# Kernel tuning notes

Hardware: AMD Instinct MI355X
Metric: run time of the kernel (lower is better)

The kernel has to match this reference:

```python
import jax, jax.numpy as jnp
import numpy as np

B, P, D = 8, 1024, 768
H = 12
HD = D // H


def setup_inputs() -> dict:
    key = jax.random.key(0)
    k1, k2, k3, k4, k5 = jax.random.split(key, 5)
    s = 0.02
    return {
        "x": jax.random.normal(k1, (B, P, D), dtype=jnp.float32),
        "w_qkv": jax.random.normal(k2, (D, 3 * D), dtype=jnp.float32) * s,
        "b_qkv": jax.random.normal(k3, (3 * D,), dtype=jnp.float32) * s,
        "w_proj": jax.random.normal(k4, (D, D), dtype=jnp.float32) * s,
        "b_proj": jax.random.normal(k5, (D,), dtype=jnp.float32) * s,
    }


def reference(x, w_qkv, b_qkv, w_proj, b_proj):
    b, p, d = x.shape
    scale = HD ** -0.5
    qkv = x @ w_qkv + b_qkv                      # [B,P,3D]
    qkv = qkv.reshape(b, p, 3, H, HD).transpose(2, 0, 3, 1, 4)  # [3,B,H,P,HD]
    q, k, v = qkv[0], qkv[1], qkv[2]
    attn = jnp.einsum("bhqd,bhkd->bhqk", q, k) * scale
    attn = jax.nn.softmax(attn, axis=-1)         # attn_drop is identity (p=0)
    weighted_avg = jnp.einsum("bhqk,bhkd->bhqd", attn, v)
    weighted_avg = weighted_avg.transpose(0, 2, 1, 3).reshape(b, p, d)  # [B,P,D]
    out = weighted_avg @ w_proj + b_proj         # proj_drop is identity (p=0)
    return (out, weighted_avg)
```

## Files before the change

### kernel.cpp

```cpp
#include <hip/hip_runtime.h>
#include <hip/hip_bf16.h>


typedef __attribute__((ext_vector_type(8))) short short8;
typedef __attribute__((ext_vector_type(4))) float f32x4;

#define MFMA_BF16(a, b, c) __builtin_amdgcn_mfma_f32_16x16x32_bf16((a), (b), (c), 0, 0, 0)

#define NB 8
#define NP 1024
#define ND 768
#define NH 12
#define NHD 64
#define NTOK (NB * NP)
#define N3D (3 * ND)
#define OUT_HALF (NTOK * ND)
#define QSCALE 0.18033688f

__device__ __forceinline__ void gload_lds16(const void* gptr, void* ldsptr) {
  __builtin_amdgcn_global_load_lds(
      (const __attribute__((address_space(1))) unsigned int*)gptr,
      (__attribute__((address_space(3))) unsigned int*)ldsptr, 16, 0, 0);
}


__global__ void k_cvt_x(const float* __restrict__ in, __hip_bfloat16* __restrict__ out) {
  int i = (blockIdx.x * 256 + threadIdx.x) * 8;
  float4 a = *(const float4*)(in + i);
  float4 b = *(const float4*)(in + i + 4);
  union { __hip_bfloat16 h[8]; uint4 u; } r;
  r.h[0] = __float2bfloat16(a.x); r.h[1] = __float2bfloat16(a.y);
  r.h[2] = __float2bfloat16(a.z); r.h[3] = __float2bfloat16(a.w);
  r.h[4] = __float2bfloat16(b.x); r.h[5] = __float2bfloat16(b.y);
  r.h[6] = __float2bfloat16(b.z); r.h[7] = __float2bfloat16(b.w);
  *(uint4*)(out + i) = r.u;
}

__global__ void k_cvt_t(const float* __restrict__ in, __hip_bfloat16* __restrict__ out,
                        int K, int N) {
  __shared__ float tile[32][33];
  int k0 = blockIdx.x * 32;
  int n0 = blockIdx.y * 32;
  int r = threadIdx.x >> 5;
  int c = threadIdx.x & 31;
#pragma unroll
  for (int i = 0; i < 4; ++i)
    tile[r + 8 * i][c] = in[(size_t)(k0 + r + 8 * i) * N + n0 + c];
  __syncthreads();
#pragma unroll
  for (int i = 0; i < 4; ++i)
    out[(size_t)(n0 + r + 8 * i) * K + k0 + c] = __float2bfloat16(tile[c][r + 8 * i]);
}


__device__ __forceinline__ void gemm_mainloop(const __hip_bfloat16* __restrict__ A,
                                              const __hip_bfloat16* __restrict__ BT,
                                              int K, int m0, int n0,
                                              __hip_bfloat16* As, __hip_bfloat16* Bs,
                                              f32x4 acc[4][4]) {
  const int tid = threadIdx.x;
  const int wid = tid >> 6, lane = tid & 63;
  const int wm = wid >> 1, wn = wid & 1;
  const int lrow = lane & 15, lk = lane >> 4;

  const int nkt = K / 32;

#define STAGE_G(kt, half)                                                \
  {                                                                      \
    const int k0s = (kt) * 32;                                           \
    _Pragma("unroll")                                                    \
    for (int t = 0; t < 2; ++t) {                                        \
      int o = (tid + t * 256) * 16;        \
      int mr = o >> 6;                    \
      int kk = (o & 63) >> 1;                   \
      gload_lds16(A + (size_t)(m0 + mr) * K + k0s + kk,                  \
                  (char*)As + (half) * 8192 + wid * 1024 + t * 4096);    \
      gload_lds16(BT + (size_t)(n0 + mr) * K + k0s + kk,                 \
                  (char*)Bs + (half) * 8192 + wid * 1024 + t * 4096);    \
    }                                                                    \
  }

  STAGE_G(0, 0);
  __syncthreads();

  for (int kt = 0; kt < nkt; ++kt) {
    const int cur = kt & 1;
    if (kt + 1 < nkt) STAGE_G(kt + 1, cur ^ 1);

    short8 af[4], bf[4];
#pragma unroll
    for (int i = 0; i < 4; ++i) {
      af[i] = *(const short8*)((const char*)As + cur * 8192 +
                               (wm * 64 + i * 16 + lrow) * 64 + lk * 16);
      bf[i] = *(const short8*)((const char*)Bs + cur * 8192 +
                               (wn * 64 + i * 16 + lrow) * 64 + lk * 16);
    }
#pragma unroll
    for (int mi = 0; mi < 4; ++mi)
#pragma unroll
      for (int ni = 0; ni < 4; ++ni)
        acc[mi][ni] = MFMA_BF16(af[mi], bf[ni], acc[mi][ni]);

    __syncthreads();
  }
#undef STAGE_G
}


__launch_bounds__(256)
__global__ void k_qkv_gemm(const __hip_bfloat16* __restrict__ A,
                           const __hip_bfloat16* __restrict__ BT,
                           const float* __restrict__ bias,
                           __hip_bfloat16* __restrict__ q_ws,
                           __hip_bfloat16* __restrict__ k_ws,
                           __hip_bfloat16* __restrict__ v_ws) {
  __shared__ __hip_bfloat16 As[2 * 128 * 32];
  __shared__ __hip_bfloat16 Bs[2 * 128 * 32];
  const int mt = blockIdx.x & 63, nt = blockIdx.x >> 6;
  const int m0 = mt * 128, n0 = nt * 128;
  const int wid = threadIdx.x >> 6, lane = threadIdx.x & 63;
  const int wm = wid >> 1, wn = wid & 1;
  const int lrow = lane & 15, lk = lane >> 4;

  f32x4 acc[4][4] = {};
  gemm_mainloop(A, BT, ND, m0, n0, As, Bs, acc);

  const int which = n0 / ND;
#pragma unroll
  for (int ni = 0; ni < 4; ++ni) {
    const int n = n0 + wn * 64 + ni * 16 + lrow;
    const float bv = bias[n];
    const int hh = (n % ND) >> 6;
    const int hd = n & 63;
#pragma unroll
    for (int mi = 0; mi < 4; ++mi) {
      const int mbase = m0 + wm * 64 + mi * 16 + lk * 4;
#pragma unroll
      for (int i = 0; i < 4; ++i) {
        const int m = mbase + i;
        const float v = acc[mi][ni][i] + bv;
        const int b = m >> 10, p = m & 1023;
        const int bh = b * NH + hh;
        if (which == 0)      q_ws[((size_t)bh * NP + p) * NHD + hd] = __float2bfloat16(v * QSCALE);
        else if (which == 1) k_ws[((size_t)bh * NP + p) * NHD + hd] = __float2bfloat16(v);
        else                 v_ws[((size_t)bh * NHD + hd) * NP + p] = __float2bfloat16(v);
      }
    }
  }
}


#define KVBLK 64

__launch_bounds__(256)
__global__ void k_attn(const __hip_bfloat16* __restrict__ q_ws,
                       const __hip_bfloat16* __restrict__ k_ws,
                       const __hip_bfloat16* __restrict__ v_ws,
                       float* __restrict__ wavg_f32,
                       __hip_bfloat16* __restrict__ wavg_bf) {
  __shared__ char smem[2 * 16384 + 4 * 2304];
  const int bh = blockIdx.y;
  const int tid = threadIdx.x;
  const int wid = tid >> 6, lane = tid & 63;
  const int lrow = lane & 15, lk = lane >> 4;
  const int q0 = blockIdx.x * 64 + wid * 16;
  char* pbuf = smem + 32768 + wid * 2304;

  const __hip_bfloat16* Qb = q_ws + (size_t)bh * NP * NHD;
  const __hip_bfloat16* Kb = k_ws + (size_t)bh * NP * NHD;
  const __hip_bfloat16* Vb = v_ws + (size_t)bh * NHD * NP;

  short8 qf0 = *(const short8*)(Qb + (size_t)(q0 + lrow) * NHD + lk * 8);
  short8 qf1 = *(const short8*)(Qb + (size_t)(q0 + lrow) * NHD + 32 + lk * 8);

  f32x4 acc[4] = {};
  float dsum[4] = {0.f, 0.f, 0.f, 0.f};

#define STAGE(buf, key0)                                                          \
  {                                                                               \
    _Pragma("unroll")                                                             \
    for (int p = 0; p < 2; ++p) {                                                 \
      const int L = p * 4096 + tid * 16;                                          \
      const int r = L >> 7;                                                       \
      const int cb = L & 127;                                                     \
      const int sc = (cb ^ ((r & 7) << 4)) >> 1;        \
      gload_lds16(Kb + (size_t)((key0) + r) * NHD + sc, (buf) + L);               \
      gload_lds16(Vb + (size_t)r * NP + (key0) + sc, (buf) + 8192 + L);           \
    }                                                                             \
  }

  char* cur = smem;
  char* nxt = smem + 16384;
  STAGE(cur, 0);
  __syncthreads();

  for (int kc = 0; kc < NP / KVBLK; ++kc) {
    if (kc < NP / KVBLK - 1) STAGE(nxt, (kc + 1) * KVBLK);

    char* Ks = cur;
    char* Vs = cur + 8192;

    f32x4 s[4];
#pragma unroll
    for (int kt = 0; kt < 4; ++kt) {
      const int row = kt * 16 + lrow;
      const int sw = (row & 7) << 4;
      short8 klo = *(const short8*)(Ks + row * 128 + ((lk * 16) ^ sw));
      short8 khi = *(const short8*)(Ks + row * 128 + ((64 + lk * 16) ^ sw));
      f32x4 z = {0.f, 0.f, 0.f, 0.f};
      s[kt] = MFMA_BF16(qf0, klo, z);
      s[kt] = MFMA_BF16(qf1, khi, s[kt]);
    }

#pragma unroll
    for (int kt = 0; kt < 4; ++kt)
#pragma unroll
      for (int i = 0; i < 4; ++i) {
        const float p = exp2f(s[kt][i]);
        dsum[i] += p;
        *(__hip_bfloat16*)(pbuf + (lk * 4 + i) * 144 + kt * 32 + lrow * 2) =
            __float2bfloat16(p);
      }

#pragma unroll
    for (int kh = 0; kh < 2; ++kh) {
      short8 a2 = *(const short8*)(pbuf + lrow * 144 + kh * 64 + lk * 16);
#pragma unroll
      for (int hdt = 0; hdt < 4; ++hdt) {
        const int row = hdt * 16 + lrow;
        short8 vf = *(const short8*)(Vs + row * 128 +
                                     ((kh * 64 + lk * 16) ^ ((row & 7) << 4)));
        acc[hdt] = MFMA_BF16(a2, vf, acc[hdt]);
      }
    }

    __syncthreads();
    char* t = cur; cur = nxt; nxt = t;
  }

#pragma unroll
  for (int i = 0; i < 4; ++i) {
#pragma unroll
    for (int off = 1; off < 16; off <<= 1)
      dsum[i] += __shfl_xor(dsum[i], off, 16);
  }
  float rd[4];
#pragma unroll
  for (int i = 0; i < 4; ++i) rd[i] = 1.0f / dsum[i];

  const int b = bh / NH, hh = bh % NH;
#pragma unroll
  for (int hdt = 0; hdt < 4; ++hdt) {
#pragma unroll
    for (int i = 0; i < 4; ++i) {
      const int qq = q0 + lk * 4 + i;
      const int col = hh * NHD + hdt * 16 + lrow;
      const float val = acc[hdt][i] * rd[i];
      const size_t o = ((size_t)b * NP + qq) * ND + col;
      wavg_f32[o] = val;
      wavg_bf[o] = __float2bfloat16(val);
    }
  }
#undef STAGE
}


__launch_bounds__(256)
__global__ void k_proj_gemm(const __hip_bfloat16* __restrict__ A,
                            const __hip_bfloat16* __restrict__ BT,
                            const float* __restrict__ bias,
                            float* __restrict__ C) {
  __shared__ __hip_bfloat16 As[2 * 128 * 32];
  __shared__ __hip_bfloat16 Bs[2 * 128 * 32];
  const int mt = blockIdx.x & 63, nt = blockIdx.x >> 6;
  const int m0 = mt * 128, n0 = nt * 128;
  const int wid = threadIdx.x >> 6, lane = threadIdx.x & 63;
  const int wm = wid >> 1, wn = wid & 1;
  const int lrow = lane & 15, lk = lane >> 4;

  f32x4 acc[4][4] = {};
  gemm_mainloop(A, BT, ND, m0, n0, As, Bs, acc);

#pragma unroll
  for (int ni = 0; ni < 4; ++ni) {
    const int n = n0 + wn * 64 + ni * 16 + lrow;
    const float bv = bias[n];
#pragma unroll
    for (int mi = 0; mi < 4; ++mi) {
      const int mbase = m0 + wm * 64 + mi * 16 + lk * 4;
#pragma unroll
      for (int i = 0; i < 4; ++i)
        C[(size_t)(mbase + i) * ND + n] = acc[mi][ni][i] + bv;
    }
  }
}


extern "C" void kernel_launch(void* const* d_in, const int* in_sizes, int n_in,
                              void* d_out, int out_size, void* d_ws, size_t ws_size,
                              hipStream_t stream) {
  const float* x      = (const float*)d_in[0];
  const float* w_qkv  = (const float*)d_in[1];
  const float* b_qkv  = (const float*)d_in[2];
  const float* w_proj = (const float*)d_in[3];
  const float* b_proj = (const float*)d_in[4];
  float* out = (float*)d_out;
  float* wavg_out = out + OUT_HALF;

  char* ws = (char*)d_ws;
  __hip_bfloat16* xbf    = (__hip_bfloat16*)(ws);
  __hip_bfloat16* wqkvT  = (__hip_bfloat16*)(ws + 12582912);
  __hip_bfloat16* wprojT = (__hip_bfloat16*)(ws + 16121856);
  __hip_bfloat16* q_ws   = (__hip_bfloat16*)(ws + 17301504);
  __hip_bfloat16* k_ws   = (__hip_bfloat16*)(ws + 29884416);
  __hip_bfloat16* v_ws   = (__hip_bfloat16*)(ws + 42467328);
  __hip_bfloat16* wavg_bf = xbf;

  k_cvt_x<<<NTOK * ND / (256 * 8), 256, 0, stream>>>(x, xbf);
  k_cvt_t<<<dim3(ND / 32, N3D / 32), 256, 0, stream>>>(w_qkv, wqkvT, ND, N3D);
  k_cvt_t<<<dim3(ND / 32, ND / 32), 256, 0, stream>>>(w_proj, wprojT, ND, ND);
  k_qkv_gemm<<<(NTOK / 128) * (N3D / 128), 256, 0, stream>>>(xbf, wqkvT, b_qkv,
                                                             q_ws, k_ws, v_ws);
  k_attn<<<dim3(NP / 64, NB * NH), 256, 0, stream>>>(q_ws, k_ws, v_ws, wavg_out, wavg_bf);
  k_proj_gemm<<<(NTOK / 128) * (ND / 128), 256, 0, stream>>>(wavg_bf, wprojT, b_proj, out);
}
```

Before: 151.7 us.

## Triple-buffer GEMM LDS staging with one barrier per k-step

Replaces the double-buffered GEMM mainloop with a three-stage LDS ring. Loads run two tiles ahead, and each iteration waits on a partial vmcnt and a single barrier instead of a full sync at both ends. This targets the global-load latency left exposed in the QKV and projection GEMMs. It raises LDS use to 48KB per block, which may lower occupancy, and it depends on the vmcnt count matching the four loads issued per stage.

New measurement: 142.8 us. 1.06x faster.

```diff
diff --git a/kernel.cpp b/kernel.cpp
--- a/kernel.cpp
+++ b/kernel.cpp
@@ -55,55 +55,63 @@
 
 __device__ __forceinline__ void gemm_mainloop(const __hip_bfloat16* __restrict__ A,
                                               const __hip_bfloat16* __restrict__ BT,
-                                              int K, int m0, int n0,
-                                              __hip_bfloat16* As, __hip_bfloat16* Bs,
+                                              int m0, int n0, char* Ls,
                                               f32x4 acc[4][4]) {
   const int tid = threadIdx.x;
   const int wid = tid >> 6, lane = tid & 63;
   const int wm = wid >> 1, wn = wid & 1;
   const int lrow = lane & 15, lk = lane >> 4;
-
-  const int nkt = K / 32;
-
-#define STAGE_G(kt, half)                                                \
+  constexpr int K = 768, NKT = K / 32;
+
+#define STAGE_G(kt, bi)                                                  \
   {                                                                      \
     const int k0s = (kt) * 32;                                           \
+    char* dst = Ls + (bi) * 16384;                                       \
     _Pragma("unroll")                                                    \
     for (int t = 0; t < 2; ++t) {                                        \
       int o = (tid + t * 256) * 16;        \
       int mr = o >> 6;                    \
       int kk = (o & 63) >> 1;                   \
       gload_lds16(A + (size_t)(m0 + mr) * K + k0s + kk,                  \
-                  (char*)As + (half) * 8192 + wid * 1024 + t * 4096);    \
+                  dst + wid * 1024 + t * 4096);                          \
       gload_lds16(BT + (size_t)(n0 + mr) * K + k0s + kk,                 \
-                  (char*)Bs + (half) * 8192 + wid * 1024 + t * 4096);    \
+                  dst + 8192 + wid * 1024 + t * 4096);                   \
     }                                                                    \
   }
 
+#define COMPUTE_T(kt)                                                          \
+  {                                                                            \
+    const char* buf = Ls + ((kt) % 3) * 16384;                                 \
+    short8 af[4], bf[4];                                                       \
+    _Pragma("unroll")                                                          \
+    for (int i = 0; i < 4; ++i) {                                              \
+      af[i] = *(const short8*)(buf + (wm * 64 + i * 16 + lrow) * 64 + lk * 16);\
+      bf[i] = *(const short8*)(buf + 8192 +                                    \
+                               (wn * 64 + i * 16 + lrow) * 64 + lk * 16);      \
+    }                                                                          \
+    _Pragma("unroll")                                                          \
+    for (int mi = 0; mi < 4; ++mi)                                             \
+      _Pragma("unroll")                                                        \
+      for (int ni = 0; ni < 4; ++ni)                                           \
+        acc[mi][ni] = MFMA_BF16(af[mi], bf[ni], acc[mi][ni]);                  \
+  }
+
   STAGE_G(0, 0);
-  __syncthreads();
-
-  for (int kt = 0; kt < nkt; ++kt) {
-    const int cur = kt & 1;
-    if (kt + 1 < nkt) STAGE_G(kt + 1, cur ^ 1);
-
-    short8 af[4], bf[4];
-#pragma unroll
-    for (int i = 0; i < 4; ++i) {
-      af[i] = *(const short8*)((const char*)As + cur * 8192 +
-                               (wm * 64 + i * 16 + lrow) * 64 + lk * 16);
-      bf[i] = *(const short8*)((const char*)Bs + cur * 8192 +
-                               (wn * 64 + i * 16 + lrow) * 64 + lk * 16);
-    }
-#pragma unroll
-    for (int mi = 0; mi < 4; ++mi)
-#pragma unroll
-      for (int ni = 0; ni < 4; ++ni)
-        acc[mi][ni] = MFMA_BF16(af[mi], bf[ni], acc[mi][ni]);
-
-    __syncthreads();
-  }
+  STAGE_G(1, 1);
+
+#pragma unroll 3
+  for (int kt = 0; kt < NKT - 1; ++kt) {
+    asm volatile("s_waitcnt vmcnt(4)" ::: "memory");
+    __builtin_amdgcn_s_barrier();
+    if (kt + 2 < NKT) STAGE_G(kt + 2, (kt + 2) % 3);
+    COMPUTE_T(kt);
+  }
+  asm volatile("s_waitcnt vmcnt(0)" ::: "memory");
+  __builtin_amdgcn_s_barrier();
+  COMPUTE_T(NKT - 1);
+
 #undef STAGE_G
+#undef COMPUTE_T
 }
 
 
@@ -114,8 +122,7 @@
                            __hip_bfloat16* __restrict__ q_ws,
                            __hip_bfloat16* __restrict__ k_ws,
                            __hip_bfloat16* __restrict__ v_ws) {
-  __shared__ __hip_bfloat16 As[2 * 128 * 32];
-  __shared__ __hip_bfloat16 Bs[2 * 128 * 32];
+  __shared__ char Ls[3 * 16384];
   const int mt = blockIdx.x & 63, nt = blockIdx.x >> 6;
   const int m0 = mt * 128, n0 = nt * 128;
   const int wid = threadIdx.x >> 6, lane = threadIdx.x & 63;
@@ -123,7 +130,7 @@
   const int lrow = lane & 15, lk = lane >> 4;
 
   f32x4 acc[4][4] = {};
-  gemm_mainloop(A, BT, ND, m0, n0, As, Bs, acc);
+  gemm_mainloop(A, BT, m0, n0, Ls, acc);
 
   const int which = n0 / ND;
 #pragma unroll
@@ -270,8 +277,7 @@
                             const __hip_bfloat16* __restrict__ BT,
                             const float* __restrict__ bias,
                             float* __restrict__ C) {
-  __shared__ __hip_bfloat16 As[2 * 128 * 32];
-  __shared__ __hip_bfloat16 Bs[2 * 128 * 32];
+  __shared__ char Ls[3 * 16384];
   const int mt = blockIdx.x & 63, nt = blockIdx.x >> 6;
   const int m0 = mt * 128, n0 = nt * 128;
   const int wid = threadIdx.x >> 6, lane = threadIdx.x & 63;
@@ -279,7 +285,7 @@
   const int lrow = lane & 15, lk = lane >> 4;
 
   f32x4 acc[4][4] = {};
-  gemm_mainloop(A, BT, ND, m0, n0, As, Bs, acc);
+  gemm_mainloop(A, BT, m0, n0, Ls, acc);
 
 #pragma unroll
   for (int ni = 0; ni < 4; ++ni) {
```
